# Kernel tuning notes

Measured on AMD Instinct MI355X. Metric: run time of the kernel, lower is better.

Reference implementation:

```python
import jax, jax.numpy as jnp
import numpy as np

IMC = 256
EPS = 1e-6
BN_EPS = 1e-5
GRID = (69.12, 79.36)      # (depth, width) in meters
OFF = (0.0, -39.68, 0.0)   # (xoff, yoff, zoff)
RES = 0.64
ZMIN, ZMAX = -3.0, 2.76
SCALES = [0.25, 0.125, 0.0625, 0.03125, 0.015625]


def make_corners():
    # replicates make_grid(): corner lattice in lidar coords, shape [nz, nx, ny, 3]
    nx = int(round(GRID[0] / RES)) + 1   # 109
    ny = int(round(GRID[1] / RES)) + 1   # 125
    nz = int(round((ZMAX - ZMIN) / RES)) + 1  # 10
    xc = RES * np.arange(nx) + OFF[0]
    yc = GRID[1] - RES * np.arange(ny) + OFF[1]
    zc = ZMAX - RES * np.arange(nz)
    xx, yy = np.meshgrid(xc, yc, indexing='ij')
    base = np.stack([xx, yy, np.full_like(xx, OFF[2])], axis=-1)  # [nx,ny,3]
    zoffs = np.stack([np.zeros(nz), np.zeros(nz), zc], axis=-1)   # [nz,3]
    corners = base[None] + zoffs[:, None, None, :]
    return jnp.asarray(corners, jnp.float32)


def grid_sample(img, grid):
    # img [B,C,H,W]; grid [B,P,N,2] xy in [-1,1]; bilinear, zero padding, align_corners=False
    B, C, H, W = img.shape
    x = (grid[..., 0] + 1.0) * (W * 0.5) - 0.5
    y = (grid[..., 1] + 1.0) * (H * 0.5) - 0.5
    x0f = jnp.floor(x); y0f = jnp.floor(y)
    wx = (x - x0f).reshape(B, 1, -1)
    wy = (y - y0f).reshape(B, 1, -1)
    x0 = x0f.astype(jnp.int32); y0 = y0f.astype(jnp.int32)
    flat = img.reshape(B, C, H * W)
    def g(xi, yi):
        ok = ((xi >= 0) & (xi < W) & (yi >= 0) & (yi < H)).reshape(B, 1, -1)
        idx = (jnp.clip(yi, 0, H - 1) * W + jnp.clip(xi, 0, W - 1)).reshape(B, 1, -1)
        return jnp.take_along_axis(flat, idx, axis=2) * ok
    v00 = g(x0, y0); v01 = g(x0 + 1, y0); v10 = g(x0, y0 + 1); v11 = g(x0 + 1, y0 + 1)
    out = (v00 * (1 - wx) + v01 * wx) * (1 - wy) + (v10 * (1 - wx) + v11 * wx) * wy
    return out.reshape(B, C, grid.shape[1], grid.shape[2])


def oft(feats, calib, corners, scale, w, b):
    B, C, Hf, Wf = feats.shape
    # perspective projection of grid corners into the image plane
    hom = jnp.einsum('bij,zdwj->bzdwi', calib[:, :, :3], corners) + calib[:, None, None, None, :, 3]
    xy = hom[..., :2] / hom[..., 2:3]                      # [B,nz,nx,ny,2]
    img_size = jnp.array([Wf, Hf], jnp.float32) / scale
    nc = jnp.clip(2.0 * xy / img_size - 1.0, -1.0, 1.0)
    mn = jnp.minimum(nc[:, :-1, :-1, :-1], nc[:, :-1, 1:, :-1])
    mx = jnp.maximum(nc[:, 1:, 1:, 1:], nc[:, 1:, :-1, 1:])
    bbox = jnp.concatenate([mn, mx], axis=-1)              # [B,Zc,Dc,Wc,4]
    _, Zc, Dc, Wc, _ = bbox.shape
    bbox = bbox.reshape(B, Zc, Dc * Wc, 4)
    area = ((bbox[..., 2] - bbox[..., 0]) * (bbox[..., 3] - bbox[..., 1])
            * (Hf * Wf * 0.25) + EPS)[:, None]             # [B,1,Zc,N]
    visible = (area > EPS).astype(feats.dtype)
    ii = jnp.cumsum(jnp.cumsum(feats, axis=-1), axis=-2)   # integral image
    tl = grid_sample(ii, jnp.stack([bbox[..., 0], bbox[..., 1]], -1))
    br = grid_sample(ii, jnp.stack([bbox[..., 2], bbox[..., 3]], -1))
    tr = grid_sample(ii, jnp.stack([bbox[..., 2], bbox[..., 1]], -1))
    bl = grid_sample(ii, jnp.stack([bbox[..., 0], bbox[..., 3]], -1))
    vox = (tl + br - tr - bl) / area * visible             # [B,C,Zc,N]
    vox = vox.transpose(0, 3, 1, 2).reshape(B * Dc * Wc, C * Zc)
    ortho = jax.nn.relu(vox @ w.T + b).reshape(B, Dc, Wc, -1)
    return ortho.transpose(0, 3, 2, 1)                     # [B,imc,Wc,Dc]


def attention(x, aw, ab):
    s = jax.nn.sigmoid(x.mean(axis=(2, 3)) @ aw.T + ab)
    return x * s[:, :, None, None]


def conv3x3(x, w, stride):
    return jax.lax.conv_general_dilated(x, w, (stride, stride), ((1, 1), (1, 1)),
                                        dimension_numbers=('NCHW', 'OIHW', 'NCHW'))


def bn(x, g, b, m, v):
    scale = g / jnp.sqrt(v + BN_EPS)
    return (x - m[None, :, None, None]) * scale[None, :, None, None] + b[None, :, None, None]


def make_calib(B):
    K = np.array([[560.0, 0.0, 640.0], [0.0, 560.0, 192.0], [0.0, 0.0, 1.0]])
    Rt = np.array([[0.0, -1.0, 0.0, 0.05],   # lidar(x fwd, y left, z up) -> cam(x right, y down, z fwd)
                   [0.0, 0.0, -1.0, -0.30],
                   [1.0, 0.0, 0.0, 0.27]])
    P = K @ Rt
    return jnp.asarray(np.tile(P[None], (B, 1, 1)), jnp.float32)


def setup_inputs() -> dict:
    key = jax.random.key(0)
    ks = jax.random.split(key, 16)
    B = 1
    shapes = [(B, IMC, 96, 320), (B, IMC, 48, 160), (B, IMC, 24, 80), (B, IMC, 12, 40), (B, IMC, 6, 20)]
    feats = [jax.random.normal(ks[i], s, jnp.float32) * 0.1 for i, s in enumerate(shapes)]
    HC = 9 * IMC  # height_channels = int((2.76-(-3))/0.64 * 256) = 2304
    inp = {
        'feats04': feats[0], 'feats08': feats[1], 'feats16': feats[2],
        'feats32': feats[3], 'feats64': feats[4],
        'calib': make_calib(B),
        'oft_w': jax.random.normal(ks[5], (5, IMC, HC), jnp.float32) * 0.02,
        'oft_b': jax.random.normal(ks[6], (5, IMC), jnp.float32) * 0.02,
        'att_w': jax.random.normal(ks[7], (IMC, IMC), jnp.float32) * 0.05,
        'att_b': jnp.zeros((IMC,), jnp.float32),
        'conv1_w': jax.random.normal(ks[8], (IMC, IMC * 5, 3, 3), jnp.float32) * 0.02,
        'bn1_g': 1.0 + 0.1 * jax.random.normal(ks[9], (IMC,), jnp.float32),
        'bn1_b': 0.05 * jax.random.normal(ks[10], (IMC,), jnp.float32),
        'bn1_m': 0.05 * jax.random.normal(ks[11], (IMC,), jnp.float32),
        'bn1_v': jax.random.uniform(ks[12], (IMC,), jnp.float32, 0.5, 1.5),
        'conv2_w': jax.random.normal(ks[13], (IMC, IMC, 3, 3), jnp.float32) * 0.02,
        'bn2_g': 1.0 + 0.1 * jax.random.normal(ks[14], (IMC,), jnp.float32),
        'bn2_b': jnp.zeros((IMC,), jnp.float32),
        'bn2_m': jnp.zeros((IMC,), jnp.float32),
        'bn2_v': jax.random.uniform(ks[15], (IMC,), jnp.float32, 0.5, 1.5),
    }
    return inp


def reference(feats04, feats08, feats16, feats32, feats64, calib,
              oft_w, oft_b, att_w, att_b,
              conv1_w, bn1_g, bn1_b, bn1_m, bn1_v,
              conv2_w, bn2_g, bn2_b, bn2_m, bn2_v):
    corners = make_corners()
    feats = [feats04, feats08, feats16, feats32, feats64]
    orthos = [attention(oft(f, calib, corners, s, oft_w[i], oft_b[i]), att_w, att_b)
              for i, (f, s) in enumerate(zip(feats, SCALES))]
    x = jnp.concatenate(orthos, axis=1)            # [B, 5*imc, 124, 108]
    x = jax.nn.relu(bn(conv3x3(x, conv1_w, 2), bn1_g, bn1_b, bn1_m, bn1_v))
    x = jax.nn.relu(bn(conv3x3(x, conv2_w, 1), bn2_g, bn2_b, bn2_m, bn2_v))
    return x                                       # [B, imc, 62, 54]
```

## Files before the change

kernel.cpp:

```cpp
#include <hip/hip_runtime.h>

typedef __attribute__((ext_vector_type(8))) short short8;
typedef __attribute__((ext_vector_type(4))) float float4v;
typedef __attribute__((ext_vector_type(4))) int int4v;
typedef __attribute__((ext_vector_type(4))) unsigned short ushort4v;

#define NBOX 13392
#define ZC 9
#define KOFT 2304
#define NPIX 3348
#define NBLK0 105
#define NBLKC 27
#define TILEK 4096
#define NBSTRIDE 294912
#define VOXSZ 30965760
#define TAPINTS 16

__device__ __forceinline__ unsigned short f2bf(float f) {
  union { float f; unsigned int i; } v; v.f = f;
  unsigned int r = v.i + 0x7FFFu + ((v.i >> 16) & 1u);
  return (unsigned short)(r >> 16);
}
__device__ __forceinline__ float bf2f(unsigned short u) {
  union { unsigned int i; float f; } v; v.i = ((unsigned int)u) << 16; return v.f;
}
__device__ __forceinline__ float i2f(int i) {
  union { int i; float f; } v; v.i = i; return v.f;
}

__device__ __constant__ int cHFs[5] = {96, 48, 24, 12, 6};
__device__ __constant__ int cWFs[5] = {320, 160, 80, 40, 20};
__device__ __constant__ size_t cIIof[5] = {0, 7864320, 9830400, 10321920, 10444800};

__device__ __forceinline__ const int* uniform_ptr(const int* p) {
  unsigned lo = (unsigned)(uintptr_t)p;
  unsigned hi = (unsigned)((uintptr_t)p >> 32);
  lo = (unsigned)__builtin_amdgcn_readfirstlane((int)lo);
  hi = (unsigned)__builtin_amdgcn_readfirstlane((int)hi);
  return (const int*)(((uintptr_t)hi << 32) | (uintptr_t)lo);
}

__device__ __forceinline__ void async16(const unsigned short* g, unsigned short* l) {
  __builtin_amdgcn_global_load_lds(
      (const __attribute__((address_space(1))) unsigned int*)g,
      (__attribute__((address_space(3))) unsigned int*)l, 16, 0, 0);
}

__global__ void k_alpha_beta(const float* __restrict__ oft_b,
                             const float* __restrict__ g1, const float* __restrict__ b1,
                             const float* __restrict__ m1, const float* __restrict__ v1,
                             const float* __restrict__ g2, const float* __restrict__ b2,
                             const float* __restrict__ m2, const float* __restrict__ v2,
                             float* __restrict__ ALPHA, float* __restrict__ BETA,
                             float* __restrict__ MEANS, unsigned short* __restrict__ ZPAGE) {
  int g = blockIdx.x, c = threadIdx.x;
  float al, be;
  if (g < 5) { al = 1.f; be = oft_b[g * 256 + c]; MEANS[g * 256 + c] = 0.f; }
  else {
    const float* gg = (g == 5) ? g1 : g2;
    const float* bb = (g == 5) ? b1 : b2;
    const float* mm = (g == 5) ? m1 : m2;
    const float* vv = (g == 5) ? v1 : v2;
    al = gg[c] / sqrtf(vv[c] + 1e-5f);
    be = bb[c] - mm[c] * al;
  }
  ALPHA[g * 256 + c] = al; BETA[g * 256 + c] = be;
  if (g == 0) ZPAGE[c] = 0;
}

__global__ void k_wpermT(const float* __restrict__ w, unsigned short* __restrict__ wp) {
  int idx = blockIdx.x * 256 + threadIdx.x;
  int sc = idx / 589824;
  int r  = idx % 589824;
  int j   = r & 7;
  int row = (r >> 3) & 127;
  int kc  = (r >> 10) & 3;
  int cs  = r >> 12;
  int cb  = cs / 72, s = cs % 72;
  int oc = cb * 128 + row;
  int k  = s * 32 + kc * 8 + j;
  int z = k >> 8, c = k & 255;
  wp[idx] = f2bf(w[((size_t)sc * 256 + oc) * 2304 + c * 9 + z]);
}

__global__ void k_wperm1T(const float* __restrict__ w, const float* __restrict__ satt,
                          unsigned short* __restrict__ wp) {
  int idx = blockIdx.x * 256 + threadIdx.x;
  int j   = idx & 7;
  int row = (idx >> 3) & 127;
  int kc  = (idx >> 10) & 3;
  int rest = idx >> 12;
  int s = rest % 40; rest /= 40;
  int r = rest % 9;  int cb = rest / 9;
  int oc = cb * 128 + row;
  int ic = s * 32 + kc * 8 + j;
  wp[idx] = f2bf(w[(size_t)oc * 11520 + ic * 9 + r] * satt[ic]);
}

__global__ void k_wperm2T(const float* __restrict__ w, unsigned short* __restrict__ wp) {
  int idx = blockIdx.x * 256 + threadIdx.x;
  int j   = idx & 7;
  int row = (idx >> 3) & 127;
  int kc  = (idx >> 10) & 3;
  int rest = idx >> 12;
  int s = rest % 8; rest /= 8;
  int r = rest % 9; int cb = rest / 9;
  int oc = cb * 128 + row;
  int ic = s * 32 + kc * 8 + j;
  wp[idx] = f2bf(w[(size_t)oc * 2304 + ic * 9 + r]);
}

__global__ void k_tapsA(const float* __restrict__ calib, int* __restrict__ taps, int s0) {
  int idx = blockIdx.x * 256 + threadIdx.x;
  if (idx >= ZC * NBOX) return;
  int slab = blockIdx.y, sc = s0 + slab;
  int Hf = cHFs[sc], Wf = cWFs[sc];
  float areaScale = (float)(Hf * Wf) * 0.25f;
  int z = idx / NBOX, n = idx % NBOX;
  int d = n / 124, wj = n % 124;
  float P[12];
#pragma unroll
  for (int i = 0; i < 12; ++i) P[i] = calib[i];
  auto proj = [&](int k, int i, int j, float& nxo, float& nyo) {
    float X = 0.64f * (float)i;
    float Y = 39.68f - 0.64f * (float)j;
    float Z = 2.76f - 0.64f * (float)k;
    float hx = P[0] * X + P[1] * Y + P[2]  * Z + P[3];
    float hy = P[4] * X + P[5] * Y + P[6]  * Z + P[7];
    float hz = P[8] * X + P[9] * Y + P[10] * Z + P[11];
    float px = hx / hz, py = hy / hz;
    nxo = 2.f * px / 1280.f - 1.f; nxo = fminf(fmaxf(nxo, -1.f), 1.f);
    nyo = 2.f * py / 384.f  - 1.f; nyo = fminf(fmaxf(nyo, -1.f), 1.f);
  };
  float ax, ay, bx, by, cx, cy, dx, dy;
  proj(z,     d,     wj,     ax, ay);
  proj(z,     d + 1, wj,     bx, by);
  proj(z + 1, d + 1, wj + 1, cx, cy);
  proj(z + 1, d,     wj + 1, dx, dy);
  float x0 = fminf(ax, bx), y0 = fminf(ay, by);
  float x1 = fmaxf(cx, dx), y1 = fmaxf(cy, dy);
  float rawA = (x1 - x0) * (y1 - y0) * areaScale;
  int* ob = taps + (size_t)slab * (ZC * NBOX * TAPINTS) + (size_t)idx * TAPINTS;
  if (!(rawA > 0.f)) { ob[0] = 0; return; }
  float inv = 1.f / (rawA + 1e-6f);

  float u0 = (x0 + 1.f) * ((float)Wf * 0.5f) - 0.5f;
  float u1 = (x1 + 1.f) * ((float)Wf * 0.5f) - 0.5f;
  float fu0 = floorf(u0), fu1 = floorf(u1);
  int cx0 = (int)fu0, cx1 = (int)fu1;
  float wx0 = u0 - fu0, wx1 = u1 - fu1;
  int xs[4]; float xw[4];
  xs[0] = cx0; xs[1] = cx0 + 1; xs[2] = cx1; xs[3] = cx1 + 1;
  xw[0] = (1.f - wx0) * inv; xw[1] = wx0 * inv;
  xw[2] = -(1.f - wx1) * inv; xw[3] = -wx1 * inv;
  int dcx = cx1 - cx0;
  if (dcx == 0)      { xw[0] += xw[2]; xw[1] += xw[3]; xw[2] = 0.f; xw[3] = 0.f; }
  else if (dcx == 1) { xw[1] += xw[2]; xw[2] = xw[3]; xs[2] = xs[3]; xw[3] = 0.f; }
#pragma unroll
  for (int j = 0; j < 4; ++j) {
    if (xs[j] < 0 || xs[j] >= Wf) xw[j] = 0.f;
    xs[j] = min(max(xs[j], 0), Wf - 1);
  }
#define CSWX(a, b) { if (xw[a] == 0.f && xw[b] != 0.f) { \
    float tw = xw[a]; xw[a] = xw[b]; xw[b] = tw; \
    int ts = xs[a]; xs[a] = xs[b]; xs[b] = ts; } }
  CSWX(0, 1) CSWX(2, 3) CSWX(0, 2) CSWX(1, 3) CSWX(1, 2)
#undef CSWX
  int nx = (xw[0] != 0.f) + (xw[1] != 0.f) + (xw[2] != 0.f) + (xw[3] != 0.f);

  float v0 = (y0 + 1.f) * ((float)Hf * 0.5f) - 0.5f;
  float v1 = (y1 + 1.f) * ((float)Hf * 0.5f) - 0.5f;
  float fv0 = floorf(v0), fv1 = floorf(v1);
  int ry0 = (int)fv0, ry1 = (int)fv1;
  float wy0 = v0 - fv0, wy1 = v1 - fv1;
  int ys[4]; float yw[4];
  ys[0] = ry0; ys[1] = ry0 + 1; ys[2] = ry1; ys[3] = ry1 + 1;
  yw[0] = 1.f - wy0; yw[1] = wy0; yw[2] = -(1.f - wy1); yw[3] = -wy1;
  int dcy = ry1 - ry0;
  if (dcy == 0)      { yw[0] += yw[2]; yw[1] += yw[3]; yw[2] = 0.f; yw[3] = 0.f; }
  else if (dcy == 1) { yw[1] += yw[2]; yw[2] = yw[3]; ys[2] = ys[3]; yw[3] = 0.f; }
#pragma unroll
  for (int j = 0; j < 4; ++j) {
    if (ys[j] < 0 || ys[j] >= Hf) yw[j] = 0.f;
    ys[j] = min(max(ys[j], 0), Hf - 1);
  }
#define CSWY(a, b) { if (yw[a] == 0.f && yw[b] != 0.f) { \
    float tw = yw[a]; yw[a] = yw[b]; yw[b] = tw; \
    int ts = ys[a]; ys[a] = ys[b]; ys[b] = ts; } }
  CSWY(0, 1) CSWY(2, 3) CSWY(0, 2) CSWY(1, 3) CSWY(1, 2)
#undef CSWY
  int ny = (yw[0] != 0.f) + (yw[1] != 0.f) + (yw[2] != 0.f) + (yw[3] != 0.f);

  if (nx == 0 || ny == 0) { ob[0] = 0; return; }

  int4v* obv = (int4v*)ob;
  obv[0] = (int4v){(xs[0] << 10) | (nx << 25) | (ny << 28),
                   xs[1] << 10, xs[2] << 10, xs[3] << 10};
  obv[1] = (int4v){ys[0] * Wf * 1024, ys[1] * Wf * 1024,
                   ys[2] * Wf * 1024, ys[3] * Wf * 1024};
  float4v* wb = (float4v*)ob;
  wb[2] = (float4v){xw[0], xw[1], xw[2], xw[3]};
  wb[3] = (float4v){yw[0], yw[1], yw[2], yw[3]};
}

__global__ void k_transpose_all(const float* __restrict__ f0, const float* __restrict__ f1,
                                const float* __restrict__ f2, const float* __restrict__ f3,
                                const float* __restrict__ f4, float* __restrict__ II) {
  int b = blockIdx.x;
  int sc, cx;
  if (b < 480)      { sc = 0; cx = b; }
  else if (b < 600) { sc = 1; cx = b - 480; }
  else if (b < 630) { sc = 2; cx = b - 600; }
  else if (b < 638) { sc = 3; cx = b - 630; }
  else              { sc = 4; cx = b - 638; }
  const int Ss[5] = {30720, 7680, 1920, 480, 120};
  const float* srcs[5] = {f0, f1, f2, f3, f4};
  int S = Ss[sc];
  const float* src = srcs[sc];
  float* dst = II + cIIof[sc];
  __shared__ float tile[64][65];
  int t = threadIdx.x;
  int wave = t >> 6, lane = t & 63;
  int s0 = cx * 64, c0 = blockIdx.y * 64;
#pragma unroll
  for (int i = 0; i < 16; ++i) {
    int c_l = wave * 16 + i;
    if (s0 + lane < S) tile[c_l][lane] = src[(size_t)(c0 + c_l) * S + s0 + lane];
  }
  __syncthreads();
#pragma unroll
  for (int i = 0; i < 16; ++i) {
    int s_l = wave * 16 + i;
    if (s0 + s_l < S) dst[(size_t)(s0 + s_l) * 256 + c0 + lane] = tile[lane][s_l];
  }
}

__global__ void k_cumw_all(float* __restrict__ II) {
  int b = blockIdx.x;
  int sc, h;
  if (b < 96)       { sc = 0; h = b; }
  else if (b < 144) { sc = 1; h = b - 96; }
  else if (b < 168) { sc = 2; h = b - 144; }
  else if (b < 180) { sc = 3; h = b - 168; }
  else              { sc = 4; h = b - 180; }
  int Wf = cWFs[sc];
  float* p = II + cIIof[sc] + (size_t)h * Wf * 256 + threadIdx.x;
  float acc = 0.f;
#pragma unroll 4
  for (int w = 0; w < Wf; ++w) { acc += p[(size_t)w * 256]; p[(size_t)w * 256] = acc; }
}

__global__ void k_cumh_all(float* __restrict__ II) {
  int b = blockIdx.x;
  int sc, w;
  if (b < 320)      { sc = 0; w = b; }
  else if (b < 480) { sc = 1; w = b - 320; }
  else if (b < 560) { sc = 2; w = b - 480; }
  else if (b < 600) { sc = 3; w = b - 560; }
  else              { sc = 4; w = b - 600; }
  const int Hfs[5] = {96, 48, 24, 12, 6};
  int Hf = Hfs[sc];
  size_t stride = (size_t)cWFs[sc] * 256;
  float* p = II + cIIof[sc] + (size_t)w * 256 + threadIdx.x;
  float acc = 0.f;
#pragma unroll 4
  for (int h = 0; h < Hf; ++h) { acc += p[h * stride]; p[h * stride] = acc; }
}

__global__ __launch_bounds__(512) void k_sampleA(const float* __restrict__ II,
                                                 const int* __restrict__ taps,
                                                 unsigned short* __restrict__ voxT,
                                                 int s0) {
  __shared__ unsigned short st[3][8][66][4];
  int t = threadIdx.x;
  int wave = t >> 6, lane = t & 63;
  int n = blockIdx.x * 8 + wave;
  int zg = blockIdx.y * 3;
  int slab = blockIdx.z, sc = s0 + slab;
  const float* ii = II + cIIof[sc];
  const int* tbase = taps + (size_t)slab * (ZC * NBOX * TAPINTS);
  unsigned short* vox = voxT + (size_t)slab * VOXSZ;
  const char* iib = (const char*)ii + (lane << 4);
#pragma unroll
  for (int dz = 0; dz < 3; ++dz) {
    int z = zg + dz;
    const int* tb = uniform_ptr(tbase + (size_t)(z * NBOX + n) * TAPINTS);
    int xo[4], yo[4]; float xw[4], yw[4];
#pragma unroll
    for (int i = 0; i < 4; ++i) xo[i] = tb[i];
#pragma unroll
    for (int i = 0; i < 4; ++i) yo[i] = tb[4 + i];
#pragma unroll
    for (int i = 0; i < 4; ++i) xw[i] = i2f(tb[8 + i]);
#pragma unroll
    for (int i = 0; i < 4; ++i) yw[i] = i2f(tb[12 + i]);
    unsigned h = (unsigned)xo[0];
    int nx = (h >> 25) & 7;
    int ny = (h >> 28) & 7;
    xo[0] = (int)(h & 0x01FFFFFFu);
    ushort4v o;
    if (ny == 0) {
      o[0] = 0; o[1] = 0; o[2] = 0; o[3] = 0;
    } else {
      int o_[16]; float w_[16];
#pragma unroll
      for (int r = 0; r < 4; ++r)
#pragma unroll
        for (int c = 0; c < 4; ++c) {
          o_[r * 4 + c] = yo[r] + xo[c];
          w_[r * 4 + c] = yw[r] * xw[c];
        }
      float4v a0 = {0.f, 0.f, 0.f, 0.f}, a1 = a0;
#define TAP(i, acc) { float4v t_ = *(const float4v*)(iib + (size_t)(unsigned)o_[i]); acc += t_ * w_[i]; }
      TAP(0, a0)
      if (nx > 1) TAP(1, a1)
      if (nx > 2) TAP(2, a0)
      if (nx > 3) TAP(3, a1)
      if (ny > 1) {
        TAP(4, a0)
        if (nx > 1) TAP(5, a1)
        if (nx > 2) TAP(6, a0)
        if (nx > 3) TAP(7, a1)
      }
      if (ny > 2) {
        TAP(8, a0)
        if (nx > 1) TAP(9, a1)
        if (nx > 2) TAP(10, a0)
        if (nx > 3) TAP(11, a1)
      }
      if (ny > 3) {
        TAP(12, a0)
        if (nx > 1) TAP(13, a1)
        if (nx > 2) TAP(14, a0)
        if (nx > 3) TAP(15, a1)
      }
#undef TAP
      float4v acc = a0 + a1;
#pragma unroll
      for (int j = 0; j < 4; ++j) o[j] = f2bf(acc[j]);
    }
    *(ushort4v*)&st[dz][wave][lane][0] = o;
  }
  __syncthreads();
  int nb = (blockIdx.x * 8) >> 7;
  int r0 = (blockIdx.x * 8) & 127;
  unsigned short* outb = vox + (size_t)nb * NBSTRIDE + (size_t)r0 * 32;
  int lane32 = t & 31;
  int row = lane32 >> 2, kc = lane32 & 3;
#pragma unroll
  for (int p = 0; p < 2; ++p) {
    int q = p * 16 + (t >> 5);
    if (q < 24) {
      int zq = q >> 3;
      int si = q & 7;
      short8 v = *(const short8*)&st[zq][row][si * 8 + kc * 2][0];
      *(short8*)(outb + (size_t)(zg + zq) * 32768 + (size_t)si * 4096
                 + (size_t)(row * 32 + kc * 8)) = v;
    }
  }
}

__global__ __launch_bounds__(256) void k_gemmT_all(
    const unsigned short* __restrict__ AT, const unsigned short* __restrict__ BT,
    const float* __restrict__ beta, unsigned short* __restrict__ xbuf, int s0) {
  __shared__ unsigned short ls[8704];
  unsigned short* lsA = ls;
  unsigned short* lsB = ls + 4096;
  int t = threadIdx.x;
  int lane = t & 63, wave = t >> 6;
  int l15 = lane & 15, quad = lane >> 4;
  int nb = blockIdx.x, cb = blockIdx.y;
  int slab = blockIdx.z, sc = s0 + slab;
  int wrow = (wave >> 1) * 64, wcol = (wave & 1) * 64;

  const unsigned short* ga = AT + (size_t)slab * VOXSZ + (size_t)nb * NBSTRIDE + t * 8;
  const unsigned short* gb = BT + (size_t)sc * 589824 + (size_t)cb * NBSTRIDE + t * 8;
  unsigned short* ldA = lsA + t * 8;
  unsigned short* ldB = lsB + t * 8;

  float4v acc[4][4];
#pragma unroll
  for (int mi = 0; mi < 4; ++mi)
#pragma unroll
    for (int ni = 0; ni < 4; ++ni) acc[mi][ni] = (float4v){0.f, 0.f, 0.f, 0.f};

  for (int s = 0; s < 72; ++s) {
    async16(ga, ldA);
    async16(ga + 2048, ldA + 2048);
    async16(gb, ldB);
    async16(gb + 2048, ldB + 2048);
    ga += TILEK; gb += TILEK;
    __syncthreads();
    short8 af[4], bf[4];
    const short8* pA = (const short8*)lsA;
    const short8* pB = (const short8*)lsB;
#pragma unroll
    for (int mi = 0; mi < 4; ++mi) af[mi] = pA[(wrow + mi * 16 + l15) * 4 + quad];
#pragma unroll
    for (int ni = 0; ni < 4; ++ni) bf[ni] = pB[quad * 128 + wcol + ni * 16 + l15];
#pragma unroll
    for (int mi = 0; mi < 4; ++mi)
#pragma unroll
      for (int ni = 0; ni < 4; ++ni)
        acc[mi][ni] = __builtin_amdgcn_mfma_f32_16x16x32_bf16(af[mi], bf[ni], acc[mi][ni], 0, 0, 0);
    __syncthreads();
  }

  float bval[4];
#pragma unroll
  for (int ni = 0; ni < 4; ++ni)
    bval[ni] = beta[sc * 256 + cb * 128 + wcol + ni * 16 + l15];
#pragma unroll
  for (int ph = 0; ph < 2; ++ph) {
    if (wrow == ph * 64) {
#pragma unroll
      for (int mi = 0; mi < 4; ++mi)
#pragma unroll
        for (int ni = 0; ni < 4; ++ni)
#pragma unroll
          for (int j = 0; j < 4; ++j) {
            int row = mi * 16 + quad * 4 + j;
            int col = wcol + ni * 16 + l15;
            float v = acc[mi][ni][j] + bval[ni];
            ls[row * 136 + col] = f2bf(v > 0.f ? v : 0.f);
          }
    }
    __syncthreads();
#pragma unroll
    for (int it = 0; it < 4; ++it) {
      int idx = it * 256 + t;
      int row = idx >> 4, ch = idx & 15;
      int nn = nb * 128 + ph * 64 + row;
      if (nn < NBOX) {
        short8 v = *(const short8*)&ls[row * 136 + ch * 8];
        *(short8*)(xbuf + (size_t)nn * 1280 + sc * 256 + cb * 128 + ch * 8) = v;
      }
    }
    __syncthreads();
  }
}

__global__ __launch_bounds__(256) void k_gemmT(
    const unsigned short* __restrict__ AT, const unsigned short* __restrict__ BT,
    float* __restrict__ part) {
  __shared__ unsigned short lsA[4096];
  __shared__ unsigned short lsB[4096];
  int t = threadIdx.x;
  int lane = t & 63, wave = t >> 6;
  int l15 = lane & 15, quad = lane >> 4;
  int nb = blockIdx.x, cb = blockIdx.y, ks = blockIdx.z;
  int wrow = (wave >> 1) * 64, wcol = (wave & 1) * 64;

  const unsigned short* ga = AT + (size_t)nb * NBSTRIDE + (size_t)ks * 18 * TILEK + t * 8;
  const unsigned short* gb = BT + (size_t)cb * NBSTRIDE + (size_t)ks * 18 * TILEK + t * 8;
  unsigned short* ldA = lsA + t * 8;
  unsigned short* ldB = lsB + t * 8;

  float4v acc[4][4];
#pragma unroll
  for (int mi = 0; mi < 4; ++mi)
#pragma unroll
    for (int ni = 0; ni < 4; ++ni) acc[mi][ni] = (float4v){0.f, 0.f, 0.f, 0.f};

  for (int s = 0; s < 18; ++s) {
    async16(ga, ldA);
    async16(ga + 2048, ldA + 2048);
    async16(gb, ldB);
    async16(gb + 2048, ldB + 2048);
    ga += TILEK; gb += TILEK;
    __syncthreads();
    short8 af[4], bf[4];
    const short8* pA = (const short8*)lsA;
    const short8* pB = (const short8*)lsB;
#pragma unroll
    for (int mi = 0; mi < 4; ++mi) af[mi] = pA[(wrow + mi * 16 + l15) * 4 + quad];
#pragma unroll
    for (int ni = 0; ni < 4; ++ni) bf[ni] = pB[quad * 128 + wcol + ni * 16 + l15];
#pragma unroll
    for (int mi = 0; mi < 4; ++mi)
#pragma unroll
      for (int ni = 0; ni < 4; ++ni)
        acc[mi][ni] = __builtin_amdgcn_mfma_f32_16x16x32_bf16(af[mi], bf[ni], acc[mi][ni], 0, 0, 0);
    __syncthreads();
  }

#pragma unroll
  for (int mi = 0; mi < 4; ++mi) {
    int nb0 = nb * 128 + wrow + mi * 16 + quad * 4;
#pragma unroll
    for (int j = 0; j < 4; ++j) {
      int nn = nb0 + j;
      if (nn < NBOX) {
#pragma unroll
        for (int ni = 0; ni < 4; ++ni) {
          int oc = cb * 128 + wcol + ni * 16 + l15;
          part[((size_t)ks * NBOX + nn) * 256 + oc] = acc[mi][ni][j];
        }
      }
    }
  }
}

__global__ void k_redoft(const float* __restrict__ part, const float* __restrict__ beta,
                         unsigned short* __restrict__ xbuf, int choff) {
  int n = blockIdx.x, oc = threadIdx.x;
  float v = part[(size_t)n * 256 + oc]
          + part[((size_t)NBOX + n) * 256 + oc]
          + part[((size_t)2 * NBOX + n) * 256 + oc]
          + part[((size_t)3 * NBOX + n) * 256 + oc];
  v += beta[oc];
  v = v > 0.f ? v : 0.f;
  xbuf[(size_t)n * 1280 + choff + oc] = f2bf(v);
}

template <int MODE>
__global__ __launch_bounds__(256) void k_gemmS(
    const unsigned short* __restrict__ A, const unsigned short* __restrict__ BT,
    float* __restrict__ part, const unsigned short* __restrict__ zpage) {
  constexpr int KIC   = (MODE == 1) ? 1280 : 256;
  constexpr int STEPS = KIC / 32;
  __shared__ unsigned short lsA[4096];
  __shared__ unsigned short lsB[4096];
  int t = threadIdx.x;
  int lane = t & 63, wave = t >> 6;
  int l15 = lane & 15, quad = lane >> 4;
  int n0 = blockIdx.x * 128, oc0 = blockIdx.y * 128;
  int r = blockIdx.z;
  int wrow = (wave >> 1) * 64, wcol = (wave & 1) * 64;
  int srow = t & 127, skc = t >> 7;

  int p = n0 + srow;
  int oy = p / 54, ox = p - oy * 54;
  int ky = r / 3, kx = r - ky * 3;
  bool valid; int sp;
  if (MODE == 1) {
    int ih = 2 * oy + ky - 1, iw = 2 * ox + kx - 1;
    valid = (p < NPIX) && ((unsigned)ih < 124u) && ((unsigned)iw < 108u);
    sp = iw * 124 + ih;
  } else {
    int ih = oy + ky - 1, iw = ox + kx - 1;
    valid = (p < NPIX) && ((unsigned)ih < 62u) && ((unsigned)iw < 54u);
    sp = ih * 54 + iw;
  }
  const unsigned short* ga = valid ? (A + (size_t)sp * KIC + skc * 8) : zpage;
  int astep = valid ? 32 : 0;
  const unsigned short* gb = BT + ((size_t)(blockIdx.y * 9 + r) * STEPS) * TILEK + t * 8;
  unsigned short* ldA = lsA + t * 8;
  unsigned short* ldB = lsB + t * 8;

  float4v acc[4][4];
#pragma unroll
  for (int mi = 0; mi < 4; ++mi)
#pragma unroll
    for (int ni = 0; ni < 4; ++ni) acc[mi][ni] = (float4v){0.f, 0.f, 0.f, 0.f};

  for (int s = 0; s < STEPS; ++s) {
    async16(ga, ldA);
    async16(ga + 16, ldA + 2048);
    async16(gb, ldB);
    async16(gb + 2048, ldB + 2048);
    ga += astep; gb += TILEK;
    __syncthreads();
    short8 af[4], bf[4];
    const short8* pA = (const short8*)lsA;
    const short8* pB = (const short8*)lsB;
#pragma unroll
    for (int mi = 0; mi < 4; ++mi) af[mi] = pA[quad * 128 + wrow + mi * 16 + l15];
#pragma unroll
    for (int ni = 0; ni < 4; ++ni) bf[ni] = pB[quad * 128 + wcol + ni * 16 + l15];
#pragma unroll
    for (int mi = 0; mi < 4; ++mi)
#pragma unroll
      for (int ni = 0; ni < 4; ++ni)
        acc[mi][ni] = __builtin_amdgcn_mfma_f32_16x16x32_bf16(af[mi], bf[ni], acc[mi][ni], 0, 0, 0);
    __syncthreads();
  }

#pragma unroll
  for (int mi = 0; mi < 4; ++mi) {
    int nb0 = n0 + wrow + mi * 16 + quad * 4;
#pragma unroll
    for (int j = 0; j < 4; ++j) {
      int nn = nb0 + j;
      if (nn < NPIX) {
#pragma unroll
        for (int ni = 0; ni < 4; ++ni) {
          int oc = oc0 + wcol + ni * 16 + l15;
          part[((size_t)r * NPIX + nn) * 256 + oc] = acc[mi][ni][j];
        }
      }
    }
  }
}

template <bool F32OUT>
__global__ void k_redconv(const float* __restrict__ part, const float* __restrict__ alpha,
                          const float* __restrict__ beta, void* __restrict__ outv) {
  int p = blockIdx.x, oc = threadIdx.x;
  float v = 0.f;
#pragma unroll
  for (int r = 0; r < 9; ++r) v += part[((size_t)r * NPIX + p) * 256 + oc];
  v = v * alpha[oc] + beta[oc];
  v = v > 0.f ? v : 0.f;
  if (F32OUT) ((float*)outv)[(size_t)oc * NPIX + p] = v;
  else ((unsigned short*)outv)[(size_t)p * 256 + oc] = f2bf(v);
}

__global__ void k_means2(const unsigned short* __restrict__ x, float* __restrict__ means) {
  int tid = threadIdx.x;
  if (tid >= 160) return;
  int c0 = tid * 8;
  int r0 = blockIdx.x * 64;
  float part[8] = {0.f, 0.f, 0.f, 0.f, 0.f, 0.f, 0.f, 0.f};
  for (int i = 0; i < 64; ++i) {
    int row = r0 + i;
    if (row < NBOX) {
      short8 v = *(const short8*)(x + (size_t)row * 1280 + c0);
#pragma unroll
      for (int j = 0; j < 8; ++j) part[j] += bf2f((unsigned short)v[j]);
    }
  }
#pragma unroll
  for (int j = 0; j < 8; ++j) atomicAdd(&means[c0 + j], part[j]);
}

__global__ void k_att(const float* __restrict__ means, const float* __restrict__ aw,
                      const float* __restrict__ ab, float* __restrict__ satt) {
  int sc = blockIdx.x, c = threadIdx.x;
  __shared__ float m[256];
  m[c] = means[sc * 256 + c] * (1.f / (float)NBOX);
  __syncthreads();
  float acc = ab[c];
  for (int j = 0; j < 256; ++j) acc += m[j] * aw[c * 256 + j];
  satt[sc * 256 + c] = 1.f / (1.f + expf(-acc));
}

extern "C" void kernel_launch(void* const* d_in, const int* in_sizes, int n_in,
                              void* d_out, int out_size, void* d_ws, size_t ws_size,
                              hipStream_t stream) {
  const float* feats[5];
  for (int i = 0; i < 5; ++i) feats[i] = (const float*)d_in[i];
  const float* calib   = (const float*)d_in[5];
  const float* oft_w   = (const float*)d_in[6];
  const float* oft_b   = (const float*)d_in[7];
  const float* att_w   = (const float*)d_in[8];
  const float* att_b   = (const float*)d_in[9];
  const float* conv1_w = (const float*)d_in[10];
  const float* bn1g = (const float*)d_in[11];
  const float* bn1b = (const float*)d_in[12];
  const float* bn1m = (const float*)d_in[13];
  const float* bn1v = (const float*)d_in[14];
  const float* conv2_w = (const float*)d_in[15];
  const float* bn2g = (const float*)d_in[16];
  const float* bn2b = (const float*)d_in[17];
  const float* bn2m = (const float*)d_in[18];
  const float* bn2v = (const float*)d_in[19];

  char* ws = (char*)d_ws;
  size_t off = 0;
  auto alloc = [&](size_t bytes) -> void* {
    void* p = ws + off; off += (bytes + 255) & ~(size_t)255; return p;
  };
  unsigned short* WPERMT = (unsigned short*)alloc((size_t)5 * 589824 * 2);
  unsigned short* WC1T   = (unsigned short*)alloc((size_t)2949120 * 2);
  unsigned short* WC2T   = (unsigned short*)alloc((size_t)589824 * 2);
  float*          II     = (float*)alloc((size_t)10475520 * 4);
  unsigned short* XBUF   = (unsigned short*)alloc((size_t)NBOX * 1280 * 2);
  unsigned short* Y1     = (unsigned short*)alloc((size_t)NPIX * 256 * 2);
  float*          MEANS  = (float*)alloc(1280 * 4);
  float*          SATT   = (float*)alloc(1280 * 4);
  float*          ALPHA  = (float*)alloc(7 * 256 * 4);
  float*          BETA   = (float*)alloc(7 * 256 * 4);
  unsigned short* ZPAGE  = (unsigned short*)alloc(256 * 2);

  const size_t SLAB    = (size_t)VOXSZ * 2;
  const size_t TAPSZ_C = (size_t)ZC * NBOX * 64;
  const size_t PARTSZ  = (size_t)4 * NBOX * 256 * 4;
  size_t rem = (ws_size > off) ? ws_size - off : 0;

  int NS;
  int* TAPS; unsigned short* VOXT; float* PART;
  if (rem >= 2 * (SLAB + TAPSZ_C)) {
    NS = (int)(rem / (SLAB + TAPSZ_C)); if (NS > 5) NS = 5;
    TAPS = (int*)alloc((size_t)NS * TAPSZ_C);
    VOXT = (unsigned short*)alloc((size_t)NS * SLAB);
    PART = (float*)VOXT;
  } else {
    NS = 0;
    VOXT = (unsigned short*)alloc(SLAB);
    PART = (float*)alloc(PARTSZ);
    TAPS = (int*)PART;
  }
  (void)in_sizes; (void)n_in; (void)out_size;

  k_alpha_beta<<<7, 256, 0, stream>>>(oft_b, bn1g, bn1b, bn1m, bn1v,
                                      bn2g, bn2b, bn2m, bn2v, ALPHA, BETA, MEANS, ZPAGE);
  k_wpermT<<<11520, 256, 0, stream>>>(oft_w, WPERMT);
  k_wperm2T<<<2304, 256, 0, stream>>>(conv2_w, WC2T);

  k_transpose_all<<<dim3(640, 4), 256, 0, stream>>>(feats[0], feats[1], feats[2],
                                                    feats[3], feats[4], II);
  k_cumw_all<<<186, 256, 0, stream>>>(II);
  k_cumh_all<<<620, 256, 0, stream>>>(II);

  const int TGRID = (ZC * NBOX + 255) / 256;
  if (NS > 0) {
    int g0 = 0;
    while (g0 < 5) {
      int gsz = 5 - g0; if (gsz > NS) gsz = NS;
      k_tapsA<<<dim3(TGRID, gsz), 256, 0, stream>>>(calib, TAPS, g0);
      k_sampleA<<<dim3(NBOX / 8, 3, gsz), 512, 0, stream>>>(II, TAPS, VOXT, g0);
      k_gemmT_all<<<dim3(NBLK0, 2, gsz), 256, 0, stream>>>(VOXT, WPERMT, BETA, XBUF, g0);
      g0 += gsz;
    }
  } else {
    for (int s = 0; s < 5; ++s) {
      k_tapsA<<<dim3(TGRID, 1), 256, 0, stream>>>(calib, TAPS, s);
      k_sampleA<<<dim3(NBOX / 8, 3, 1), 512, 0, stream>>>(II, TAPS, VOXT, s);
      k_gemmT<<<dim3(NBLK0, 2, 4), 256, 0, stream>>>(
          VOXT, WPERMT + (size_t)s * 589824, PART);
      k_redoft<<<NBOX, 256, 0, stream>>>(PART, BETA + s * 256, XBUF, s * 256);
    }
  }

  k_means2<<<(NBOX + 63) / 64, 256, 0, stream>>>(XBUF, MEANS);
  k_att<<<5, 256, 0, stream>>>(MEANS, att_w, att_b, SATT);
  k_wperm1T<<<11520, 256, 0, stream>>>(conv1_w, SATT, WC1T);

  k_gemmS<1><<<dim3(NBLKC, 2, 9), 256, 0, stream>>>(XBUF, WC1T, PART, ZPAGE);
  k_redconv<false><<<NPIX, 256, 0, stream>>>(PART, ALPHA + 5 * 256, BETA + 5 * 256, Y1);

  k_gemmS<2><<<dim3(NBLKC, 2, 9), 256, 0, stream>>>(Y1, WC2T, PART, ZPAGE);
  k_redconv<true><<<NPIX, 256, 0, stream>>>(PART, ALPHA + 6 * 256, BETA + 6 * 256, d_out);
}
```

Before: 797.1 us.

## Fuse channel means into OFT GEMM, coalesce weight permutes, batch tap computation

Weight-permute kernels now read source weights in coalesced rows, one block per output channel, and scatter to the permuted bf16 layout instead of gathering with strided reads. The per-channel mean reduction is folded into the OFT GEMM epilogue using shared-memory and global atomics, which removes the separate k_means2 pass over XBUF in the slab path. When the workspace is large enough, taps for all five scales are computed in one launch up front. Atomic float accumulation makes the mean summation order nondeterministic.

New measurement: 746.1 us. 1.07x faster.

```diff
diff --git a/kernel.cpp b/kernel.cpp
--- a/kernel.cpp
+++ b/kernel.cpp
@@ -69,45 +69,54 @@
 }
 
 __global__ void k_wpermT(const float* __restrict__ w, unsigned short* __restrict__ wp) {
-  int idx = blockIdx.x * 256 + threadIdx.x;
-  int sc = idx / 589824;
-  int r  = idx % 589824;
-  int j   = r & 7;
-  int row = (r >> 3) & 127;
-  int kc  = (r >> 10) & 3;
-  int cs  = r >> 12;
-  int cb  = cs / 72, s = cs % 72;
-  int oc = cb * 128 + row;
-  int k  = s * 32 + kc * 8 + j;
-  int z = k >> 8, c = k & 255;
-  wp[idx] = f2bf(w[((size_t)sc * 256 + oc) * 2304 + c * 9 + z]);
+  int b = blockIdx.x;
+  int sc = b >> 8, oc = b & 255;
+  int t = threadIdx.x;
+  const float* src = w + (size_t)b * 2304;
+  int row = oc & 127, cb = oc >> 7;
+  unsigned short* dst = wp + (size_t)sc * 589824 + (size_t)cb * 294912 + row * 8;
+#pragma unroll
+  for (int i = 0; i < 9; ++i) {
+    int idx = i * 256 + t;
+    float v = src[idx];
+    int c = idx / 9, z = idx - c * 9;
+    int k = z * 256 + c;
+    int s = k >> 5, kc = (k >> 3) & 3, j = k & 7;
+    dst[(size_t)s * 4096 + kc * 1024 + j] = f2bf(v);
+  }
 }
 
 __global__ void k_wperm1T(const float* __restrict__ w, const float* __restrict__ satt,
                           unsigned short* __restrict__ wp) {
-  int idx = blockIdx.x * 256 + threadIdx.x;
-  int j   = idx & 7;
-  int row = (idx >> 3) & 127;
-  int kc  = (idx >> 10) & 3;
-  int rest = idx >> 12;
-  int s = rest % 40; rest /= 40;
-  int r = rest % 9;  int cb = rest / 9;
-  int oc = cb * 128 + row;
-  int ic = s * 32 + kc * 8 + j;
-  wp[idx] = f2bf(w[(size_t)oc * 11520 + ic * 9 + r] * satt[ic]);
+  int oc = blockIdx.x;
+  int t = threadIdx.x;
+  const float* src = w + (size_t)oc * 11520;
+  int row = oc & 127, cb = oc >> 7;
+  unsigned short* dst = wp + (size_t)cb * (9 * 40 * 4096) + row * 8;
+#pragma unroll
+  for (int i = 0; i < 45; ++i) {
+    int idx = i * 256 + t;
+    float v = src[idx];
+    int ic = idx / 9, r = idx - ic * 9;
+    int s = ic >> 5, kc = (ic >> 3) & 3, j = ic & 7;
+    dst[(size_t)(r * 40 + s) * 4096 + kc * 1024 + j] = f2bf(v * satt[ic]);
+  }
 }
 
 __global__ void k_wperm2T(const float* __restrict__ w, unsigned short* __restrict__ wp) {
-  int idx = blockIdx.x * 256 + threadIdx.x;
-  int j   = idx & 7;
-  int row = (idx >> 3) & 127;
-  int kc  = (idx >> 10) & 3;
-  int rest = idx >> 12;
-  int s = rest % 8; rest /= 8;
-  int r = rest % 9; int cb = rest / 9;
-  int oc = cb * 128 + row;
-  int ic = s * 32 + kc * 8 + j;
-  wp[idx] = f2bf(w[(size_t)oc * 2304 + ic * 9 + r]);
+  int oc = blockIdx.x;
+  int t = threadIdx.x;
+  const float* src = w + (size_t)oc * 2304;
+  int row = oc & 127, cb = oc >> 7;
+  unsigned short* dst = wp + (size_t)cb * (9 * 8 * 4096) + row * 8;
+#pragma unroll
+  for (int i = 0; i < 9; ++i) {
+    int idx = i * 256 + t;
+    float v = src[idx];
+    int ic = idx / 9, r = idx - ic * 9;
+    int s = ic >> 5, kc = (ic >> 3) & 3, j = ic & 7;
+    dst[(size_t)(r * 8 + s) * 4096 + kc * 1024 + j] = f2bf(v);
+  }
 }
 
 __global__ void k_tapsA(const float* __restrict__ calib, int* __restrict__ taps, int s0) {
@@ -362,8 +371,10 @@
 
 __global__ __launch_bounds__(256) void k_gemmT_all(
     const unsigned short* __restrict__ AT, const unsigned short* __restrict__ BT,
-    const float* __restrict__ beta, unsigned short* __restrict__ xbuf, int s0) {
+    const float* __restrict__ beta, unsigned short* __restrict__ xbuf,
+    float* __restrict__ means, int s0) {
   __shared__ unsigned short ls[8704];
+  __shared__ float lsm[128];
   unsigned short* lsA = ls;
   unsigned short* lsB = ls + 4096;
   int t = threadIdx.x;
@@ -407,6 +418,7 @@
   }
 
   float bval[4];
+  float msum[4] = {0.f, 0.f, 0.f, 0.f};
 #pragma unroll
   for (int ni = 0; ni < 4; ++ni)
     bval[ni] = beta[sc * 256 + cb * 128 + wcol + ni * 16 + l15];
@@ -422,7 +434,9 @@
             int row = mi * 16 + quad * 4 + j;
             int col = wcol + ni * 16 + l15;
             float v = acc[mi][ni][j] + bval[ni];
-            ls[row * 136 + col] = f2bf(v > 0.f ? v : 0.f);
+            v = v > 0.f ? v : 0.f;
+            ls[row * 136 + col] = f2bf(v);
+            if (nb * 128 + wrow + row < NBOX) msum[ni] += v;
           }
     }
     __syncthreads();
@@ -438,6 +452,13 @@
     }
     __syncthreads();
   }
+  if (t < 128) lsm[t] = 0.f;
+  __syncthreads();
+#pragma unroll
+  for (int ni = 0; ni < 4; ++ni)
+    atomicAdd(&lsm[wcol + ni * 16 + l15], msum[ni]);
+  __syncthreads();
+  if (t < 128) atomicAdd(&means[sc * 256 + cb * 128 + t], lsm[t]);
 }
 
 __global__ __launch_bounds__(256) void k_gemmT(
@@ -678,15 +699,22 @@
   const size_t PARTSZ  = (size_t)4 * NBOX * 256 * 4;
   size_t rem = (ws_size > off) ? ws_size - off : 0;
 
-  int NS;
+  int NS, NT;
   int* TAPS; unsigned short* VOXT; float* PART;
-  if (rem >= 2 * (SLAB + TAPSZ_C)) {
+  if (rem >= 2 * SLAB + 5 * TAPSZ_C) {
+    NT = 5;
+    TAPS = (int*)alloc(5 * TAPSZ_C);
+    NS = (int)((rem - 5 * TAPSZ_C) / SLAB); if (NS > 5) NS = 5;
+    VOXT = (unsigned short*)alloc((size_t)NS * SLAB);
+    PART = (float*)VOXT;
+  } else if (rem >= 2 * (SLAB + TAPSZ_C)) {
+    NT = 0;
     NS = (int)(rem / (SLAB + TAPSZ_C)); if (NS > 5) NS = 5;
     TAPS = (int*)alloc((size_t)NS * TAPSZ_C);
     VOXT = (unsigned short*)alloc((size_t)NS * SLAB);
     PART = (float*)VOXT;
   } else {
-    NS = 0;
+    NS = 0; NT = 0;
     VOXT = (unsigned short*)alloc(SLAB);
     PART = (float*)alloc(PARTSZ);
     TAPS = (int*)PART;
@@ -695,8 +723,8 @@
 
   k_alpha_beta<<<7, 256, 0, stream>>>(oft_b, bn1g, bn1b, bn1m, bn1v,
                                       bn2g, bn2b, bn2m, bn2v, ALPHA, BETA, MEANS, ZPAGE);
-  k_wpermT<<<11520, 256, 0, stream>>>(oft_w, WPERMT);
-  k_wperm2T<<<2304, 256, 0, stream>>>(conv2_w, WC2T);
+  k_wpermT<<<1280, 256, 0, stream>>>(oft_w, WPERMT);
+  k_wperm2T<<<256, 256, 0, stream>>>(conv2_w, WC2T);
 
   k_transpose_all<<<dim3(640, 4), 256, 0, stream>>>(feats[0], feats[1], feats[2],
                                                     feats[3], feats[4], II);
@@ -705,12 +733,17 @@
 
   const int TGRID = (ZC * NBOX + 255) / 256;
   if (NS > 0) {
+    if (NT == 5)
+      k_tapsA<<<dim3(TGRID, 5), 256, 0, stream>>>(calib, TAPS, 0);
     int g0 = 0;
     while (g0 < 5) {
       int gsz = 5 - g0; if (gsz > NS) gsz = NS;
-      k_tapsA<<<dim3(TGRID, gsz), 256, 0, stream>>>(calib, TAPS, g0);
-      k_sampleA<<<dim3(NBOX / 8, 3, gsz), 512, 0, stream>>>(II, TAPS, VOXT, g0);
-      k_gemmT_all<<<dim3(NBLK0, 2, gsz), 256, 0, stream>>>(VOXT, WPERMT, BETA, XBUF, g0);
+      int* tg = TAPS;
+      if (NT == 5) tg = TAPS + (size_t)g0 * (ZC * NBOX * TAPINTS);
+      else k_tapsA<<<dim3(TGRID, gsz), 256, 0, stream>>>(calib, TAPS, g0);
+      k_sampleA<<<dim3(NBOX / 8, 3, gsz), 512, 0, stream>>>(II, tg, VOXT, g0);
+      k_gemmT_all<<<dim3(NBLK0, 2, gsz), 256, 0, stream>>>(VOXT, WPERMT, BETA,
+                                                           XBUF, MEANS, g0);
       g0 += gsz;
     }
   } else {
@@ -721,11 +754,11 @@
           VOXT, WPERMT + (size_t)s * 589824, PART);
       k_redoft<<<NBOX, 256, 0, stream>>>(PART, BETA + s * 256, XBUF, s * 256);
     }
-  }
-
-  k_means2<<<(NBOX + 63) / 64, 256, 0, stream>>>(XBUF, MEANS);
+    k_means2<<<(NBOX + 63) / 64, 256, 0, stream>>>(XBUF, MEANS);
+  }
+
   k_att<<<5, 256, 0, stream>>>(MEANS, att_w, att_b, SATT);
-  k_wperm1T<<<11520, 256, 0, stream>>>(conv1_w, SATT, WC1T);
+  k_wperm1T<<<256, 256, 0, stream>>>(conv1_w, SATT, WC1T);
 
   k_gemmS<1><<<dim3(NBLKC, 2, 9), 256, 0, stream>>>(XBUF, WC1T, PART, ZPAGE);
   k_redconv<false><<<NPIX, 256, 0, stream>>>(PART, ALPHA + 5 * 256, BETA + 5 * 256, Y1);
```
